# Performance work log

Measured on AMD Instinct MI355X. Metric: run time of the kernel, lower is better.

## Reference

```python
import jax, jax.numpy as jnp
import numpy as np

STEPS_PER_DAY = 144
HEADS = 4
MODEL_D = 152  # 24 input + 24 tod + 24 dow + 80 adaptive
HEAD_D = MODEL_D // HEADS
FF_D = 256
L = 12
PRED = 12
N = 358
B = 16
EVT_D = 1024
HID_EVT = 256
NUM_EVT = 4096
KMAX = 8
NEG = -1e30


def _layer_norm(x, g, b, eps=1e-5):
    m = jnp.mean(x, -1, keepdims=True)
    v = jnp.mean((x - m) ** 2, -1, keepdims=True)
    return (x - m) * jax.lax.rsqrt(v + eps) * g + b


def _mha(x, Wq, bq, Wk, bk, Wv, bv, Wo, bo):
    # x: (B, A, S, D); self-attention over axis S
    b_, a_, s_, d_ = x.shape
    q = (x @ Wq + bq).reshape(b_, a_, s_, HEADS, HEAD_D)
    k = (x @ Wk + bk).reshape(b_, a_, s_, HEADS, HEAD_D)
    v = (x @ Wv + bv).reshape(b_, a_, s_, HEADS, HEAD_D)
    scores = jnp.einsum('baqhd,bakhd->bahqk', q, k) * (HEAD_D ** -0.5)
    attn = jax.nn.softmax(scores, axis=-1)
    out = jnp.einsum('bahqk,bakhd->baqhd', attn, v).reshape(b_, a_, s_, d_)
    return out @ Wo + bo


def setup_inputs() -> dict:
    key = jax.random.key(0)
    ks = jax.random.split(key, 24)
    f32 = jnp.float32

    def nrm(k, shape, s=0.02):
        return jax.random.normal(k, shape, dtype=f32) * s

    inp = {}
    inp['var_x'] = jax.random.normal(ks[0], (B, L, N, 1), dtype=f32)
    inp['marker_x'] = jax.random.uniform(ks[1], (B, L, N, 4), dtype=f32)
    inp['W_in'] = nrm(ks[2], (3, 24)); inp['b_in'] = jnp.zeros((24,), f32)
    inp['tod_emb'] = nrm(ks[3], (STEPS_PER_DAY, 24))
    inp['dow_emb'] = nrm(ks[4], (7, 24))
    inp['adaptive_emb'] = nrm(ks[5], (L, N, 80))
    inp['Wq'] = nrm(ks[6], (6, MODEL_D, MODEL_D)); inp['bq'] = jnp.zeros((6, MODEL_D), f32)
    inp['Wk'] = nrm(ks[7], (6, MODEL_D, MODEL_D)); inp['bk'] = jnp.zeros((6, MODEL_D), f32)
    inp['Wv'] = nrm(ks[8], (6, MODEL_D, MODEL_D)); inp['bv'] = jnp.zeros((6, MODEL_D), f32)
    inp['Wo'] = nrm(ks[9], (6, MODEL_D, MODEL_D)); inp['bo'] = jnp.zeros((6, MODEL_D), f32)
    inp['W1'] = nrm(ks[10], (6, MODEL_D, FF_D)); inp['b1'] = jnp.zeros((6, FF_D), f32)
    inp['W2'] = nrm(ks[11], (6, FF_D, MODEL_D)); inp['b2'] = jnp.zeros((6, MODEL_D), f32)
    inp['ln1_g'] = jnp.ones((6, MODEL_D), f32); inp['ln1_b'] = jnp.zeros((6, MODEL_D), f32)
    inp['ln2_g'] = jnp.ones((6, MODEL_D), f32); inp['ln2_b'] = jnp.zeros((6, MODEL_D), f32)
    inp['event_embeddings'] = nrm(ks[12], (NUM_EVT + 1, EVT_D)).at[0].set(0.0)
    inp['W_evt'] = nrm(ks[13], (EVT_D, HID_EVT)); inp['b_evt'] = jnp.zeros((HID_EVT,), f32)
    inp['W_mm'] = nrm(ks[14], (L * (MODEL_D + HID_EVT), PRED)); inp['b_mm'] = jnp.zeros((PRED,), f32)
    inp['W_ts'] = nrm(ks[15], (L * MODEL_D, PRED)); inp['b_ts'] = jnp.zeros((PRED,), f32)
    inp['doy_indices'] = jax.random.randint(ks[16], (366, KMAX), 1, NUM_EVT + 1, dtype=jnp.int32)
    mask = jax.random.uniform(ks[17], (366, KMAX)) < 0.6
    inp['doy_mask'] = mask.at[:, 0].set(True)
    return inp


def reference(var_x, marker_x, W_in, b_in, tod_emb, dow_emb, adaptive_emb,
              Wq, bq, Wk, bk, Wv, bv, Wo, bo, W1, b1, W2, b2,
              ln1_g, ln1_b, ln2_g, ln2_b, event_embeddings, W_evt, b_evt,
              W_mm, b_mm, W_ts, b_ts, doy_indices, doy_mask):
    b_, l_, n_, _ = var_x.shape
    tod = jnp.clip((marker_x[..., 0] * STEPS_PER_DAY).astype(jnp.int32), 0, STEPS_PER_DAY - 1)
    dow = jnp.clip((marker_x[..., 1] * 7).astype(jnp.int32), 0, 6)
    x_in = jnp.concatenate([var_x, marker_x[..., 0:1], marker_x[..., 1:2]], axis=-1)
    x = jnp.concatenate([
        x_in @ W_in + b_in,
        tod_emb[tod],
        dow_emb[dow],
        jnp.broadcast_to(adaptive_emb[None], (b_, l_, n_, adaptive_emb.shape[-1])),
    ], axis=-1)  # (B, L, N, MODEL_D)
    # 3 temporal attention layers (over L), then 3 spatial (over N)
    for i in range(6):
        temporal = i < 3
        h = jnp.swapaxes(x, 1, 2) if temporal else x
        out = _mha(h, Wq[i], bq[i], Wk[i], bk[i], Wv[i], bv[i], Wo[i], bo[i])
        h = _layer_norm(h + out, ln1_g[i], ln1_b[i])
        ff = jax.nn.relu(h @ W1[i] + b1[i]) @ W2[i] + b2[i]
        h = _layer_norm(h + ff, ln2_g[i], ln2_b[i])
        x = jnp.swapaxes(h, 1, 2) if temporal else h
    ts_emb = jnp.swapaxes(x, 1, 2)  # (B, N, L, D)
    # ragged event gather + linear + masked max-pool (one vectorized pass)
    doy = jnp.clip((marker_x[:, -1, 0, 3] * 365).astype(jnp.int32), 0, 365)
    idx = doy_indices[doy]           # (B, KMAX)
    msk = doy_mask[doy]              # (B, KMAX)
    h_evt = event_embeddings[idx] @ W_evt + b_evt  # (B, KMAX, HID_EVT)
    evt = jnp.max(jnp.where(msk[..., None], h_evt, NEG), axis=1)  # (B, HID_EVT)
    evt_b = jnp.broadcast_to(evt[:, None, None, :], (b_, n_, l_, HID_EVT))
    fused = jnp.concatenate([evt_b, ts_emb], axis=-1).reshape(b_, n_, -1)
    mm_pred = fused @ W_mm + b_mm
    ts_pred = ts_emb.reshape(b_, n_, -1) @ W_ts + b_ts
    return jnp.swapaxes(mm_pred + ts_pred, 1, 2)  # (B, PRED, N)
```

## Files before the change

### kernel.cpp

```cpp
#include <hip/hip_runtime.h>
#include <hip/hip_bf16.h>

using bf = __hip_bfloat16;

#define B_   16
#define L_   12
#define N_   358
#define D_   152
#define TOK_ (B_*L_*N_)
#define FF_  256
#define HD_  38
#define SCALE_ 0.16222142113076254f
#define C2_   0.23403921469340696f

__device__ __forceinline__ float bf2f(bf x) { return __bfloat162float(x); }
__device__ __forceinline__ bf f2bf(float f) { return __float2bfloat16(f); }
__device__ __forceinline__ float lo_bf(unsigned u) { return __uint_as_float(u << 16); }
__device__ __forceinline__ float hi_bf(unsigned u) { return __uint_as_float(u & 0xffff0000u); }
__device__ __forceinline__ unsigned pk_bf(float a, float b) {
  union { bf h; unsigned short u; } A, Bu;
  A.h = f2bf(a); Bu.h = f2bf(b);
  return ((unsigned)Bu.u << 16) | A.u;
}

using short8  = __attribute__((ext_vector_type(8))) short;
using float4v = __attribute__((ext_vector_type(4))) float;

__device__ __forceinline__ void gl_lds16(const void* g, void* l) {
  __builtin_amdgcn_global_load_lds(
      (const __attribute__((address_space(1))) void*)g,
      (__attribute__((address_space(3))) void*)l, 16, 0, 0);
}

template<int SUBCB>
__device__ __forceinline__ void issue_w8(const char* gsrc, ushort* lds, int w, int lane) {
  constexpr int TB = SUBCB >> 10;
  constexpr int TAIL = SUBCB & 1023;
#pragma unroll
  for (int blk0 = 0; blk0 < TB; blk0 += 8) {
    int blk = blk0 + w;
    if (blk < TB)
      gl_lds16(gsrc + blk*1024 + (size_t)lane*16, (char*)lds + blk*1024);
  }
  if (TAIL) {
    if (w == (TB & 7) && lane < TAIL/16)
      gl_lds16(gsrc + TB*1024 + (size_t)lane*16, (char*)lds + TB*1024);
  }
}

__device__ __forceinline__ short8 ld_g8(const ushort* p) {
  union { unsigned u[4]; short8 v; } t;
  t.u[0] = *(const unsigned*)(p);
  t.u[1] = *(const unsigned*)(p + 2);
  t.u[2] = *(const unsigned*)(p + 4);
  t.u[3] = *(const unsigned*)(p + 6);
  return t.v;
}

__global__ void k_beacon(float* out, int n, float val) {
  int i = blockIdx.x * 256 + threadIdx.x;
  if (i < n) out[i] = val;
}

__global__ __launch_bounds__(256) void k_embed2(
    const float* __restrict__ var_x, const float* __restrict__ marker,
    const float* __restrict__ W_in, const float* __restrict__ b_in,
    const float* __restrict__ tod_emb, const float* __restrict__ dow_emb,
    const float* __restrict__ adap, bf* __restrict__ x) {
  int t = blockIdx.x * 256 + threadIdx.x;
  if (t >= TOK_) return;
  int n = t % N_;
  int l = (t / N_) % L_;
  float var = var_x[t];
  float m0 = marker[t*4 + 0];
  float m1 = marker[t*4 + 1];
  int tod = (int)(m0 * 144.f); tod = tod < 0 ? 0 : (tod > 143 ? 143 : tod);
  int dw  = (int)(m1 * 7.f);   dw  = dw  < 0 ? 0 : (dw  > 6   ? 6   : dw);
  bf* xp = x + (long)t * D_;
  for (int d = 0; d < 24; ++d)
    xp[d] = f2bf(var * W_in[d] + m0 * W_in[24 + d] + m1 * W_in[48 + d] + b_in[d]);
  for (int d = 0; d < 24; ++d) xp[24 + d] = f2bf(tod_emb[tod*24 + d]);
  for (int d = 0; d < 24; ++d) xp[48 + d] = f2bf(dow_emb[dw*24 + d]);
  for (int d = 0; d < 80; ++d) xp[72 + d] = f2bf(adap[(l*N_ + n)*80 + d]);
}

__global__ __launch_bounds__(256) void k_wprep6(
    const float* __restrict__ Wq, const float* __restrict__ Wk,
    const float* __restrict__ Wv, const float* __restrict__ Wo,
    const float* __restrict__ W1, const float* __restrict__ W2,
    unsigned* __restrict__ out) {
  int i = blockIdx.x * 256 + threadIdx.x;
  if (i >= 6*115200) return;
  int layer = i / 115200, r = i % 115200;
  const float* src; int K, Nd, d, up, c;
  if (r < 48000) {
    c = r / 9600; int rr = r % 9600; int m = rr / 3200; int r2 = rr % 3200;
    d = r2 / 20; up = r2 % 20;
    src = (m == 0 ? Wq : (m == 1 ? Wk : Wv)) + layer*23104; K = 152; Nd = 152;
  } else if (r < 64000) {
    int rr = r - 48000; c = rr / 3200; int r2 = rr % 3200;
    d = r2 / 20; up = r2 % 20;
    src = Wo + layer*23104; K = 152; Nd = 152;
  } else if (r < 89600) {
    int rr = r - 64000; c = rr / 5120; int r2 = rr % 5120;
    d = r2 / 20; up = r2 % 20;
    src = W1 + layer*38912; K = 152; Nd = 256;
  } else {
    int rr = r - 89600; c = rr / 3200; int r2 = rr % 3200;
    d = r2 / 20; up = r2 % 20;
    src = W2 + layer*38912; K = 256; Nd = 152;
  }
  float v0 = 0.f, v1 = 0.f;
  int k0 = 32*c + 2*up;
  if (up < 16 && d < Nd) {
    if (k0 < K)     v0 = src[(long)k0*Nd + d];
    if (k0 + 1 < K) v1 = src[(long)(k0+1)*Nd + d];
  }
  out[i] = pk_bf(v0, v1);
}

template<int K, int Nd, int NW, int TOKB, int CSPLIT, bool RELU, bool LN>
__global__ __launch_bounds__(512) void k_gemm7(
    const bf* __restrict__ X, const ushort* __restrict__ Wg,
    const float* __restrict__ bi0, const float* __restrict__ bi1,
    const float* __restrict__ bi2, const bf* __restrict__ Res,
    const float* __restrict__ g, const float* __restrict__ bb,
    bf* __restrict__ Y0, bf* __restrict__ Y1, bf* __restrict__ Y2) {
  constexpr int NJ   = (Nd + 15) / 16;
  constexpr int NdP  = NJ * 16;
  constexpr int KC   = (K + 31) / 32;
  constexpr int G    = NW * CSPLIT;
  constexpr int S    = KC * G;
  constexpr int IR   = NdP / CSPLIT;
  constexpr int SUB_USH = IR * 40;
  constexpr int SUBCB   = SUB_USH * 2;
  constexpr int NJW  = IR / 32;
  constexpr int MR   = TOKB / 64;
  constexpr bool GLX = (K == 152);
  constexpr int XSTR = GLX ? K : (K + 8);
  __shared__ __align__(16) ushort Xs[TOKB * XSTR + 8];
  __shared__ __align__(16) ushort Wb[2 * SUB_USH];
  long row0 = (long)blockIdx.x * TOKB;
  int tid = threadIdx.x;
  int lane = tid & 63, w = tid >> 6;
  int cl = lane & 15, gr = lane >> 4;
  int wr = w >> 1, wc = w & 1;
  if constexpr (GLX) {
    constexpr int TBX = TOKB * K * 2 / 1024;
    const char* Xgc = (const char*)(X + row0 * K);
#pragma unroll
    for (int b0 = 0; b0 < TBX; b0 += 8) {
      int blk = b0 + w;
      if (blk < TBX)
        gl_lds16(Xgc + blk*1024 + (size_t)lane*16, (char*)Xs + blk*1024);
    }
  } else {
    const char* Xgc = (const char*)(X + row0 * K);
    for (int i = tid; i < TOKB*(K/8); i += 512) {
      int r = i / (K/8), c = i % (K/8);
      *(short8*)&Xs[r*XSTR + 8*c] = *(const short8*)(Xgc + r*(K*2) + c*16);
    }
  }
  const char* gW = (const char*)Wg;
  issue_w8<SUBCB>(gW, Wb, w, lane);
  __syncthreads();
  float4v acc[G][MR][NJW];
#pragma unroll
  for (int gi = 0; gi < G; ++gi)
#pragma unroll
    for (int mi = 0; mi < MR; ++mi)
#pragma unroll
      for (int j = 0; j < NJW; ++j) acc[gi][mi][j] = (float4v){0.f,0.f,0.f,0.f};
#pragma unroll
  for (int s = 0; s < S; ++s) {
    if (s + 1 < S)
      issue_w8<SUBCB>(gW + (size_t)(s+1)*SUBCB, Wb + ((s+1)&1)*SUB_USH, w, lane);
    int kc = (s / G) * 32;
    const ushort* wb = Wb + (s&1)*SUB_USH;
    short8 af[MR];
#pragma unroll
    for (int mi = 0; mi < MR; ++mi)
      af[mi] = *(const short8*)&Xs[((TOKB/4)*wr + 16*mi + cl)*XSTR + kc + 8*gr];
#pragma unroll
    for (int j = 0; j < NJW; ++j) {
      short8 bv = *(const short8*)&wb[((IR/2)*wc + 16*j + cl)*40 + 8*gr];
#pragma unroll
      for (int mi = 0; mi < MR; ++mi)
        acc[s % G][mi][j] =
            __builtin_amdgcn_mfma_f32_16x16x32_bf16(af[mi], bv, acc[s % G][mi][j], 0, 0, 0);
    }
    __syncthreads();
  }
  if constexpr (!LN) {
#pragma unroll
    for (int gi = 0; gi < G; ++gi) {
      bf* Y = (NW > 1) ? (gi == 0 ? Y0 : (gi == 1 ? Y1 : Y2)) : Y0;
      const float* bp = (NW > 1) ? (gi == 0 ? bi0 : (gi == 1 ? bi1 : bi2)) : bi0;
      int colb = (CSPLIT > 1 ? IR*gi : 0) + (IR/2)*wc;
#pragma unroll
      for (int j = 0; j < NJW; ++j) {
        int col = colb + 16*j + cl;
        if (col < Nd) {
          float bvs = bp[col];
#pragma unroll
          for (int mi = 0; mi < MR; ++mi) {
            long rw = row0 + (TOKB/4)*wr + 16*mi + 4*gr;
#pragma unroll
            for (int r = 0; r < 4; ++r) {
              float val = acc[gi][mi][j][r] + bvs;
              if (RELU) val = fmaxf(val, 0.f);
              Y[(rw + r) * Nd + col] = f2bf(val);
            }
          }
        }
      }
    }
  } else {
    float* LNb = (float*)Wb;
    int colb = (IR/2)*wc;
#pragma unroll
    for (int j = 0; j < NJW; ++j) {
      int col = colb + 16*j + cl;
      if (col < Nd) {
        float bvs = bi0[col];
#pragma unroll
        for (int mi = 0; mi < MR; ++mi) {
          long rw = row0 + (TOKB/4)*wr + 16*mi + 4*gr;
#pragma unroll
          for (int r = 0; r < 4; ++r)
            acc[0][mi][j][r] += bvs + bf2f(Res[(rw + r) * Nd + col]);
        }
      }
    }
    float mean[MR][4], rs[MR][4];
#pragma unroll
    for (int mi = 0; mi < MR; ++mi)
#pragma unroll
      for (int r = 0; r < 4; ++r) {
        float s = 0.f;
#pragma unroll
        for (int j = 0; j < NJW; ++j) s += acc[0][mi][j][r];
        s += __shfl_xor(s, 1, 64); s += __shfl_xor(s, 2, 64);
        s += __shfl_xor(s, 4, 64); s += __shfl_xor(s, 8, 64);
        if (cl == 0) LNb[((wr*MR + mi)*2 + wc)*16 + 4*gr + r] = s;
      }
    __syncthreads();
#pragma unroll
    for (int mi = 0; mi < MR; ++mi)
#pragma unroll
      for (int r = 0; r < 4; ++r) {
        float tot = LNb[((wr*MR + mi)*2 + 0)*16 + 4*gr + r]
                  + LNb[((wr*MR + mi)*2 + 1)*16 + 4*gr + r];
        mean[mi][r] = tot * (1.f / (float)Nd);
      }
#pragma unroll
    for (int mi = 0; mi < MR; ++mi)
#pragma unroll
      for (int r = 0; r < 4; ++r) {
        float s2 = 0.f;
#pragma unroll
        for (int j = 0; j < NJW; ++j) {
          int col = colb + 16*j + cl;
          if (col < Nd) {
            float dv = acc[0][mi][j][r] - mean[mi][r];
            s2 += dv*dv;
          }
        }
        s2 += __shfl_xor(s2, 1, 64); s2 += __shfl_xor(s2, 2, 64);
        s2 += __shfl_xor(s2, 4, 64); s2 += __shfl_xor(s2, 8, 64);
        if (cl == 0) LNb[256 + ((wr*MR + mi)*2 + wc)*16 + 4*gr + r] = s2;
      }
    __syncthreads();
#pragma unroll
    for (int mi = 0; mi < MR; ++mi)
#pragma unroll
      for (int r = 0; r < 4; ++r) {
        float tot2 = LNb[256 + ((wr*MR + mi)*2 + 0)*16 + 4*gr + r]
                   + LNb[256 + ((wr*MR + mi)*2 + 1)*16 + 4*gr + r];
        rs[mi][r] = rsqrtf(tot2 * (1.f / (float)Nd) + 1e-5f);
      }
#pragma unroll
    for (int j = 0; j < NJW; ++j) {
      int col = colb + 16*j + cl;
      if (col < Nd) {
        float gv = g[col], bv2 = bb[col];
#pragma unroll
        for (int mi = 0; mi < MR; ++mi) {
          long rw = row0 + (TOKB/4)*wr + 16*mi + 4*gr;
#pragma unroll
          for (int r = 0; r < 4; ++r)
            Y0[(rw + r) * Nd + col] =
                f2bf((acc[0][mi][j][r] - mean[mi][r]) * rs[mi][r] * gv + bv2);
        }
      }
    }
  }
}

__global__ __launch_bounds__(256) void k_attn_t2(
    const ushort* __restrict__ qg, const ushort* __restrict__ kg,
    const ushort* __restrict__ vg, bf* __restrict__ a) {
  int id = blockIdx.x; int b = id / N_; int n = id % N_;
  __shared__ ushort Ksh[4][16][40];
  __shared__ ushort Qsh[4][16][40];
  __shared__ ushort Vth[4][40][16];
  int tid = threadIdx.x;
  for (int i = tid; i < 1280; i += 256) {
    ((unsigned*)Ksh)[i] = 0u; ((unsigned*)Qsh)[i] = 0u; ((unsigned*)Vth)[i] = 0u;
  }
  __syncthreads();
  for (int i = tid; i < 4*12*19; i += 256) {
    int h = i / 228, r = i % 228, l = r / 19, t2 = r % 19;
    long off = ((long)(b*L_ + l) * N_ + n) * D_ + h*HD_ + 2*t2;
    *(unsigned*)&Ksh[h][l][2*t2] = *(const unsigned*)(kg + off);
    *(unsigned*)&Qsh[h][l][2*t2] = *(const unsigned*)(qg + off);
  }
  for (int i = tid; i < 4*12*19; i += 256) {
    int h = i / 228, r = i % 228, l = r / 19, t2 = r % 19;
    long off = ((long)(b*L_ + l) * N_ + n) * D_ + h*HD_ + 2*t2;
    unsigned u = *(const unsigned*)(vg + off);
    Vth[h][2*t2][l]     = (ushort)(u & 0xffffu);
    Vth[h][2*t2 + 1][l] = (ushort)(u >> 16);
  }
  __syncthreads();
  int lane = tid & 63, w = tid >> 6;
  int cl = lane & 15, gr = lane >> 4;
  const short8 z8 = {0,0,0,0,0,0,0,0};
  short8 a00 = *(const short8*)&Ksh[w][cl][8*gr];
  short8 qB0 = *(const short8*)&Qsh[w][cl][8*gr];
  short8 a01 = (gr == 0) ? *(const short8*)&Ksh[w][cl][32] : z8;
  short8 qB1 = (gr == 0) ? *(const short8*)&Qsh[w][cl][32] : z8;
  float4v sa = (float4v){0,0,0,0};
  sa = __builtin_amdgcn_mfma_f32_16x16x32_bf16(a00, qB0, sa, 0, 0, 0);
  sa = __builtin_amdgcn_mfma_f32_16x16x32_bf16(a01, qB1, sa, 0, 0, 0);
  float p[4];
#pragma unroll
  for (int r = 0; r < 4; ++r) {
    float xv = (4*gr + r < 12) ? sa[r]*C2_ : -1e30f;
    p[r] = __builtin_exp2f(fminf(xv, 80.f));
  }
  float sum_ = (p[0] + p[1]) + (p[2] + p[3]);
  sum_ += __shfl_xor(sum_, 16, 64);
  sum_ += __shfl_xor(sum_, 32, 64);
  unsigned u0 = pk_bf(p[0], p[1]);
  unsigned u1 = pk_bf(p[2], p[3]);
  int srcA = cl + 32*(gr & 1);
  int srcB = srcA + 16;
  unsigned w0 = __shfl(u0, srcA, 64), w1 = __shfl(u1, srcA, 64);
  unsigned w2 = __shfl(u0, srcB, 64), w3 = __shfl(u1, srcB, 64);
  union { unsigned u[4]; short8 v; } pbu;
  bool gv = gr < 2;
  pbu.u[0] = gv ? w0 : 0u; pbu.u[1] = gv ? w1 : 0u;
  pbu.u[2] = gv ? w2 : 0u; pbu.u[3] = gv ? w3 : 0u;
  short8 pB = pbu.v;
  float4v accO[3];
#pragma unroll
  for (int dt = 0; dt < 3; ++dt) {
    short8 aV = (gv && (dt < 2 || cl < 8))
        ? *(const short8*)&Vth[w][16*dt + cl][8*gr] : z8;
    accO[dt] = (float4v){0,0,0,0};
    accO[dt] = __builtin_amdgcn_mfma_f32_16x16x32_bf16(aV, pB, accO[dt], 0, 0, 0);
  }
  if (cl < 12) {
    float inv = 1.f / sum_;
    bf* ap = a + ((long)(b*L_ + cl) * N_ + n) * D_ + w*HD_;
#pragma unroll
    for (int dt = 0; dt < 2; ++dt) {
      *(unsigned*)(ap + 16*dt + 4*gr)     = pk_bf(accO[dt][0]*inv, accO[dt][1]*inv);
      *(unsigned*)(ap + 16*dt + 4*gr + 2) = pk_bf(accO[dt][2]*inv, accO[dt][3]*inv);
    }
    if (gr == 0) {
      *(unsigned*)(ap + 32) = pk_bf(accO[2][0]*inv, accO[2][1]*inv);
      *(unsigned*)(ap + 34) = pk_bf(accO[2][2]*inv, accO[2][3]*inv);
    } else if (gr == 1) {
      *(unsigned*)(ap + 36) = pk_bf(accO[2][0]*inv, accO[2][1]*inv);
    }
  }
}

__global__ __launch_bounds__(512) void k_attn_s6(
    const ushort* __restrict__ qg, const ushort* __restrict__ kg,
    const ushort* __restrict__ vg, bf* __restrict__ a) {
  __shared__ ushort Ks[360][40];
  __shared__ ushort Vt[38][392];
  int tid = threadIdx.x;
  int lane = tid & 63, w = tid >> 6;
  int cl = lane & 15, gr = lane >> 4;
  bool g0 = (gr == 0);
  const short8 z8 = {0,0,0,0,0,0,0,0};

  for (int uu = 0; uu < 2; ++uu) {
    int id = blockIdx.x * 2 + uu;
    int h = id & 3; int s = id >> 2;
    int b = s / L_; int l = s % L_;
    long base = (long)(b*L_ + l) * N_;
    if (uu) __syncthreads();
    for (int i = tid; i < 360*20; i += 512) {
      int j = i / 20, t2 = i % 20;
      unsigned u = 0u;
      if (j < N_ && t2 < 19)
        u = *(const unsigned*)(kg + (base + j)*D_ + h*HD_ + 2*t2);
      *(unsigned*)&Ks[j][2*t2] = u;
    }
    for (int i = tid; i < N_*19; i += 512) {
      int j = i / 19, t2 = i % 19;
      unsigned u = *(const unsigned*)(vg + (base + j)*D_ + h*HD_ + 2*t2);
      Vt[2*t2][j]     = (ushort)(u & 0xffffu);
      Vt[2*t2 + 1][j] = (ushort)(u >> 16);
    }
    for (int i = tid; i < 38*26; i += 512)
      Vt[i / 26][N_ + i % 26] = 0;
    __syncthreads();

    for (int qt = w; qt < 23; qt += 8) {
      const ushort* qp = qg + (base + 16*qt + cl) * D_ + h*HD_;
      short8 qB0 = ld_g8(qp + 8*gr);
      short8 qB1 = ld_g8(qp + 32 + 8*gr);
      float sum_ = 0.f;
      float4v accO[3];
      accO[0] = (float4v){0,0,0,0};
      accO[1] = (float4v){0,0,0,0};
      accO[2] = (float4v){0,0,0,0};
#pragma unroll 1
      for (int pr = 0; pr < 11; ++pr) {
        int k0 = 32*pr;
        int kr0 = k0 + cl;
        int kr1 = k0 + 16 + cl;
        float4v s0a = (float4v){0,0,0,0}, s1a = (float4v){0,0,0,0};
        {
          short8 a00 = *(const short8*)&Ks[kr0][8*gr];
          short8 a10 = *(const short8*)&Ks[kr1][8*gr];
          __builtin_amdgcn_s_setprio(1);
          s0a = __builtin_amdgcn_mfma_f32_16x16x32_bf16(a00, qB0, s0a, 0, 0, 0);
          s1a = __builtin_amdgcn_mfma_f32_16x16x32_bf16(a10, qB0, s1a, 0, 0, 0);
          short8 a01 = g0 ? *(const short8*)&Ks[kr0][32] : z8;
          short8 a11 = g0 ? *(const short8*)&Ks[kr1][32] : z8;
          s0a = __builtin_amdgcn_mfma_f32_16x16x32_bf16(a01, qB1, s0a, 0, 0, 0);
          s1a = __builtin_amdgcn_mfma_f32_16x16x32_bf16(a11, qB1, s1a, 0, 0, 0);
          __builtin_amdgcn_s_setprio(0);
        }
        float p0[4], p1[4];
#pragma unroll
        for (int r = 0; r < 4; ++r) {
          p0[r] = __builtin_exp2f(fminf(s0a[r]*C2_, 80.f));
          p1[r] = __builtin_exp2f(fminf(s1a[r]*C2_, 80.f));
        }
        sum_ += (p0[0] + p0[1]) + (p0[2] + p0[3])
              + (p1[0] + p1[1]) + (p1[2] + p1[3]);
        unsigned u0 = pk_bf(p0[0], p0[1]);
        unsigned u1 = pk_bf(p0[2], p0[3]);
        unsigned u2 = pk_bf(p1[0], p1[1]);
        unsigned u3 = pk_bf(p1[2], p1[3]);
        int srcA = cl + 16*((2*gr) & 3);
        int srcB = srcA + 16;
        unsigned a0 = __shfl(u0, srcA, 64), b0 = __shfl(u1, srcA, 64);
        unsigned c0 = __shfl(u0, srcB, 64), d0 = __shfl(u1, srcB, 64);
        unsigned a2 = __shfl(u2, srcA, 64), b2 = __shfl(u3, srcA, 64);
        unsigned c2 = __shfl(u2, srcB, 64), d2 = __shfl(u3, srcB, 64);
        bool lo = gr < 2;
        union { unsigned u[4]; short8 v; } pbu;
        pbu.u[0] = lo ? a0 : a2;
        pbu.u[1] = lo ? b0 : b2;
        pbu.u[2] = lo ? c0 : c2;
        pbu.u[3] = lo ? d0 : d2;
        short8 pB = pbu.v;
        __builtin_amdgcn_s_setprio(1);
#pragma unroll
        for (int dt = 0; dt < 3; ++dt) {
          short8 aV = (dt < 2 || cl < 6)
              ? *(const short8*)&Vt[16*dt + cl][k0 + 8*gr] : z8;
          accO[dt] = __builtin_amdgcn_mfma_f32_16x16x32_bf16(aV, pB, accO[dt], 0, 0, 0);
        }
        __builtin_amdgcn_s_setprio(0);
      }
      {
        int k0 = 352;
        int kr0 = k0 + cl; if (kr0 > 359) kr0 = 359;
        float4v s0a = (float4v){0,0,0,0};
        {
          short8 a00 = *(const short8*)&Ks[kr0][8*gr];
          s0a = __builtin_amdgcn_mfma_f32_16x16x32_bf16(a00, qB0, s0a, 0, 0, 0);
          short8 a01 = g0 ? *(const short8*)&Ks[kr0][32] : z8;
          s0a = __builtin_amdgcn_mfma_f32_16x16x32_bf16(a01, qB1, s0a, 0, 0, 0);
        }
        float p0[4];
#pragma unroll
        for (int r = 0; r < 4; ++r) {
          float xv = (4*gr + r < 6) ? s0a[r]*C2_ : -1e30f;
          p0[r] = __builtin_exp2f(fminf(xv, 80.f));
        }
        sum_ += (p0[0] + p0[1]) + (p0[2] + p0[3]);
        unsigned u0 = pk_bf(p0[0], p0[1]);
        unsigned u1 = pk_bf(p0[2], p0[3]);
        int srcA = cl + 16*((2*gr) & 3);
        int srcB = srcA + 16;
        unsigned a0 = __shfl(u0, srcA, 64), b0 = __shfl(u1, srcA, 64);
        unsigned c0 = __shfl(u0, srcB, 64), d0 = __shfl(u1, srcB, 64);
        bool lo = gr < 2;
        union { unsigned u[4]; short8 v; } pbu;
        pbu.u[0] = lo ? a0 : 0u;
        pbu.u[1] = lo ? b0 : 0u;
        pbu.u[2] = lo ? c0 : 0u;
        pbu.u[3] = lo ? d0 : 0u;
        short8 pB = pbu.v;
#pragma unroll
        for (int dt = 0; dt < 3; ++dt) {
          short8 aV = (dt < 2 || cl < 6)
              ? *(const short8*)&Vt[16*dt + cl][k0 + 8*gr] : z8;
          accO[dt] = __builtin_amdgcn_mfma_f32_16x16x32_bf16(aV, pB, accO[dt], 0, 0, 0);
        }
      }
      sum_ += __shfl_xor(sum_, 16, 64);
      sum_ += __shfl_xor(sum_, 32, 64);
      int qi = 16*qt + cl;
      if (qi < N_) {
        float inv = 1.f / sum_;
        bf* ap = a + (base + qi)*D_ + h*HD_;
#pragma unroll
        for (int dt = 0; dt < 2; ++dt) {
          *(unsigned*)(ap + 16*dt + 4*gr)     = pk_bf(accO[dt][0]*inv, accO[dt][1]*inv);
          *(unsigned*)(ap + 16*dt + 4*gr + 2) = pk_bf(accO[dt][2]*inv, accO[dt][3]*inv);
        }
        if (gr == 0) {
          *(unsigned*)(ap + 32) = pk_bf(accO[2][0]*inv, accO[2][1]*inv);
          *(unsigned*)(ap + 34) = pk_bf(accO[2][2]*inv, accO[2][3]*inv);
        } else if (gr == 1) {
          *(unsigned*)(ap + 36) = pk_bf(accO[2][0]*inv, accO[2][1]*inv);
        }
      }
    }
  }
}

__global__ __launch_bounds__(256) void k_wcomb(
    const float* __restrict__ W_mm, const float* __restrict__ W_ts,
    float* __restrict__ wcomb, float* __restrict__ wevtsum) {
  int i = blockIdx.x * 256 + threadIdx.x;
  if (i < 1824*12) {
    int r = i / 12, p = i % 12, l = r / 152, d = r % 152;
    wcomb[i] = W_mm[(l*408 + 256 + d)*12 + p] + W_ts[i];
  }
  if (i < 256*12) {
    int e = i / 12, p = i % 12;
    float s = 0.f;
    for (int l = 0; l < 12; ++l) s += W_mm[(l*408 + e)*12 + p];
    wevtsum[i] = s;
  }
}

__global__ __launch_bounds__(256) void k_evt1(
    const float* __restrict__ marker, const int* __restrict__ doy_idx,
    const float* __restrict__ emb, const float* __restrict__ W_evt,
    const float* __restrict__ b_evt, float* __restrict__ evt_h) {
  int bk = blockIdx.x; int b = bk >> 3; int ks = bk & 7;
  float m3 = marker[((b*L_ + (L_-1))*N_ + 0)*4 + 3];
  int doy = (int)(m3 * 365.f); doy = doy < 0 ? 0 : (doy > 365 ? 365 : doy);
  int idx = doy_idx[doy*8 + ks];
  if (idx < 0 || idx > 4096) idx = 0;
  int d = threadIdx.x;
  float acc = b_evt[d];
  const float* er = emb + (long)idx * 1024;
  for (int e = 0; e < 1024; ++e)
    acc += er[e] * W_evt[e*256 + d];
  evt_h[bk*256 + d] = acc;
}

__global__ __launch_bounds__(256) void k_evtpool(
    const float* __restrict__ marker, const void* __restrict__ doy_mask,
    const float* __restrict__ evt_h, float* __restrict__ evtp) {
  __shared__ int hasF32, hasBig;
  if (threadIdx.x == 0) { hasF32 = 0; hasBig = 0; }
  __syncthreads();
  const unsigned* mw = (const unsigned*)doy_mask;
  for (int w = threadIdx.x; w < 732; w += 256) {
    unsigned u = mw[w];
    if (u == 0x3F800000u) hasF32 = 1;
    else if (u > 1u) hasBig = 1;
  }
  __syncthreads();
  int fmt = hasF32 ? 2 : (hasBig ? 1 : 0);
  int b = blockIdx.x;
  float m3 = marker[((b*L_ + (L_-1))*N_ + 0)*4 + 3];
  int doy = (int)(m3 * 365.f); doy = doy < 0 ? 0 : (doy > 365 ? 365 : doy);
  int j = threadIdx.x;
  float mx = -1e30f;
  for (int kx = 0; kx < 8; ++kx) {
    bool mk;
    if (fmt == 2)      mk = ((const float*)doy_mask)[doy*8 + kx] != 0.f;
    else if (fmt == 1) mk = ((const unsigned char*)doy_mask)[doy*8 + kx] != 0;
    else               mk = ((const int*)doy_mask)[doy*8 + kx] != 0;
    if (mk) mx = fmaxf(mx, evt_h[(b*8 + kx)*256 + j]);
  }
  evtp[b*256 + j] = mx;
}

__global__ __launch_bounds__(192) void k_final3(
    const bf* __restrict__ x, const float* __restrict__ wcomb,
    const float* __restrict__ wevtsum, const float* __restrict__ evtp,
    const float* __restrict__ b_mm, const float* __restrict__ b_ts,
    float* __restrict__ out) {
  int id = blockIdx.x; int b = id / N_; int n = id % N_;
  __shared__ float xs[1824];
  __shared__ float part[16][12];
  int tid = threadIdx.x;
  for (int e = tid; e < 1824; e += 192) {
    int l = e / 152, d = e % 152;
    xs[e] = bf2f(x[((long)(b*L_ + l) * N_ + n) * 152 + d]);
  }
  __syncthreads();
  int g2 = tid / 12, p = tid % 12;
  float acc = 0.f;
  for (int e = g2; e < 1824; e += 16)
    acc += xs[e] * wcomb[e*12 + p];
  part[g2][p] = acc;
  __syncthreads();
  if (tid < 12) {
    float s = b_mm[tid] + b_ts[tid];
    for (int e = 0; e < 256; ++e) s += evtp[b*256 + e] * wevtsum[e*12 + tid];
    for (int gg = 0; gg < 16; ++gg) s += part[gg][tid];
    out[(b*12 + tid) * N_ + n] = s;
  }
}

extern "C" void kernel_launch(void* const* d_in, const int* in_sizes, int n_in,
                              void* d_out, int out_size, void* d_ws, size_t ws_size,
                              hipStream_t stream) {
  static const int expect[32] = {
    68736, 274944, 72, 24, 3456, 168, 343680,
    138624, 912, 138624, 912, 138624, 912, 138624, 912,
    233472, 1536, 233472, 912,
    912, 912, 912, 912,
    4195328, 262144, 256,
    58752, 12, 21888, 12,
    2928, 2928 };
  int nb = (out_size + 255)/256;
  if (n_in != 32) {
    k_beacon<<<nb, 256, 0, stream>>>((float*)d_out, out_size, 998.f);
    return;
  }
  for (int i = 0; i < 32; ++i) {
    if (in_sizes[i] != expect[i]) {
      k_beacon<<<nb, 256, 0, stream>>>((float*)d_out, out_size, 1000.f + i);
      return;
    }
  }
  if (out_size != 68736) {
    k_beacon<<<nb, 256, 0, stream>>>((float*)d_out, out_size, 997.f);
    return;
  }

  const float* var_x  = (const float*)d_in[0];
  const float* marker = (const float*)d_in[1];
  const float* W_in   = (const float*)d_in[2];
  const float* b_in   = (const float*)d_in[3];
  const float* tod    = (const float*)d_in[4];
  const float* dow    = (const float*)d_in[5];
  const float* adap   = (const float*)d_in[6];
  const float* Wq = (const float*)d_in[7];  const float* bq = (const float*)d_in[8];
  const float* Wk = (const float*)d_in[9];  const float* bk = (const float*)d_in[10];
  const float* Wv = (const float*)d_in[11]; const float* bv = (const float*)d_in[12];
  const float* Wo = (const float*)d_in[13]; const float* bo = (const float*)d_in[14];
  const float* W1 = (const float*)d_in[15]; const float* b1 = (const float*)d_in[16];
  const float* W2 = (const float*)d_in[17]; const float* b2 = (const float*)d_in[18];
  const float* g1 = (const float*)d_in[19]; const float* be1 = (const float*)d_in[20];
  const float* g2 = (const float*)d_in[21]; const float* be2 = (const float*)d_in[22];
  const float* emb   = (const float*)d_in[23];
  const float* W_evt = (const float*)d_in[24]; const float* b_evt = (const float*)d_in[25];
  const float* W_mm  = (const float*)d_in[26]; const float* b_mm  = (const float*)d_in[27];
  const float* W_ts  = (const float*)d_in[28]; const float* b_ts  = (const float*)d_in[29];
  const int* doyi = (const int*)d_in[30];
  const void* doym = d_in[31];

  const long TD = (long)TOK_ * D_;
  size_t need = (size_t)TD * 2 * 5
              + (size_t)(32768 + 4096 + 3072 + 21888) * 4
              + 2764800
              + 4096;
  if (ws_size < need) {
    k_beacon<<<nb, 256, 0, stream>>>((float*)d_out, out_size, (float)(ws_size >> 20));
    return;
  }

  bf* x = (bf*)d_ws;
  bf* q = x + TD;
  bf* k = q + TD;
  bf* v = k + TD;
  bf* a = v + TD;
  float* evt_h   = (float*)(a + TD);
  float* evtp    = evt_h + 32768;
  float* wevtsum = evtp + 4096;
  float* wcomb   = wevtsum + 3072;
  ushort* wprep  = (ushort*)(wcomb + 21888);

  k_wprep6<<<2700, 256, 0, stream>>>(Wq, Wk, Wv, Wo, W1, W2, (unsigned*)wprep);
  k_embed2<<<(TOK_ + 255)/256, 256, 0, stream>>>(var_x, marker, W_in, b_in,
                                                 tod, dow, adap, x);
  for (int i = 0; i < 6; ++i) {
    const ushort* pl = wprep + (size_t)i * 230400;
    k_gemm7<152,152,3,64,1,false,false><<<TOK_/64, 512, 0, stream>>>(
        x, pl, bq + i*152, bk + i*152, bv + i*152,
        nullptr, nullptr, nullptr, q, k, v);
    if (i < 3)
      k_attn_t2<<<B_*N_, 256, 0, stream>>>(
          (const ushort*)q, (const ushort*)k, (const ushort*)v, a);
    else
      k_attn_s6<<<B_*L_*2, 512, 0, stream>>>(
          (const ushort*)q, (const ushort*)k, (const ushort*)v, a);
    k_gemm7<152,152,1,128,1,false,true><<<TOK_/128, 512, 0, stream>>>(
        a, pl + 96000, bo + i*152, nullptr, nullptr,
        x, g1 + i*152, be1 + i*152, k, nullptr, nullptr);
    k_gemm7<152,256,1,128,2,true,false><<<TOK_/128, 512, 0, stream>>>(
        k, pl + 128000, b1 + i*256, nullptr, nullptr,
        nullptr, nullptr, nullptr, v, nullptr, nullptr);
    k_gemm7<256,152,1,64,1,false,true><<<TOK_/64, 512, 0, stream>>>(
        v, pl + 179200, b2 + i*152, nullptr, nullptr,
        k, g2 + i*152, be2 + i*152, x, nullptr, nullptr);
  }
  k_evt1<<<16*8, 256, 0, stream>>>(marker, doyi, emb, W_evt, b_evt, evt_h);
  k_evtpool<<<16, 256, 0, stream>>>(marker, doym, evt_h, evtp);
  k_wcomb<<<(1824*12 + 255)/256, 256, 0, stream>>>(W_mm, W_ts, wcomb, wevtsum);
  k_final3<<<B_*N_, 192, 0, stream>>>(x, wcomb, wevtsum, evtp, b_mm, b_ts,
                                      (float*)d_out);
}
```

Before: 1.188 ms.

## Fuse FFN up and down GEMMs into one kernel and merge prep kernels

Adds a fused FFN kernel that computes relu(X W1 + b1) into LDS, then the W2 GEMM with residual add and LayerNorm, so the 256-wide hidden activation never goes to global memory. Merges weight prep, embedding, event projection and output-weight combine into a single launch, and vectorises the bf16 loads in the final projection. This cuts HBM traffic and launch count, at the cost of higher LDS use per block, which may lower occupancy.

```diff
diff --git a/kernel.cpp b/kernel.cpp
--- a/kernel.cpp
+++ b/kernel.cpp
@@ -22,6 +22,9 @@
   A.h = f2bf(a); Bu.h = f2bf(b);
   return ((unsigned)Bu.u << 16) | A.u;
 }
+__device__ __forceinline__ ushort f2bf_u(float f) {
+  union { bf h; ushort u; } t; t.h = f2bf(f); return t.u;
+}
 
 using short8  = __attribute__((ext_vector_type(8))) short;
 using float4v = __attribute__((ext_vector_type(4))) float;
@@ -62,34 +65,18 @@
   if (i < n) out[i] = val;
 }
 
-__global__ __launch_bounds__(256) void k_embed2(
-    const float* __restrict__ var_x, const float* __restrict__ marker,
-    const float* __restrict__ W_in, const float* __restrict__ b_in,
-    const float* __restrict__ tod_emb, const float* __restrict__ dow_emb,
-    const float* __restrict__ adap, bf* __restrict__ x) {
-  int t = blockIdx.x * 256 + threadIdx.x;
-  if (t >= TOK_) return;
-  int n = t % N_;
-  int l = (t / N_) % L_;
-  float var = var_x[t];
-  float m0 = marker[t*4 + 0];
-  float m1 = marker[t*4 + 1];
-  int tod = (int)(m0 * 144.f); tod = tod < 0 ? 0 : (tod > 143 ? 143 : tod);
-  int dw  = (int)(m1 * 7.f);   dw  = dw  < 0 ? 0 : (dw  > 6   ? 6   : dw);
-  bf* xp = x + (long)t * D_;
-  for (int d = 0; d < 24; ++d)
-    xp[d] = f2bf(var * W_in[d] + m0 * W_in[24 + d] + m1 * W_in[48 + d] + b_in[d]);
-  for (int d = 0; d < 24; ++d) xp[24 + d] = f2bf(tod_emb[tod*24 + d]);
-  for (int d = 0; d < 24; ++d) xp[48 + d] = f2bf(dow_emb[dw*24 + d]);
-  for (int d = 0; d < 80; ++d) xp[72 + d] = f2bf(adap[(l*N_ + n)*80 + d]);
-}
-
-__global__ __launch_bounds__(256) void k_wprep6(
+#define WPREP_B 2700
+#define EMB_B   269
+#define EVT_B   128
+#define WC_B    86
+#define PREP_B  (WPREP_B + EMB_B + EVT_B + WC_B)
+
+__device__ void d_wprep(int bid, int tid,
     const float* __restrict__ Wq, const float* __restrict__ Wk,
     const float* __restrict__ Wv, const float* __restrict__ Wo,
     const float* __restrict__ W1, const float* __restrict__ W2,
     unsigned* __restrict__ out) {
-  int i = blockIdx.x * 256 + threadIdx.x;
+  int i = bid * 256 + tid;
   if (i >= 6*115200) return;
   int layer = i / 115200, r = i % 115200;
   const float* src; int K, Nd, d, up, c;
@@ -117,6 +104,81 @@
     if (k0 + 1 < K) v1 = src[(long)(k0+1)*Nd + d];
   }
   out[i] = pk_bf(v0, v1);
+}
+
+__device__ void d_embed(int bid, int tid,
+    const float* __restrict__ var_x, const float* __restrict__ marker,
+    const float* __restrict__ W_in, const float* __restrict__ b_in,
+    const float* __restrict__ tod_emb, const float* __restrict__ dow_emb,
+    const float* __restrict__ adap, bf* __restrict__ x) {
+  int t = bid * 256 + tid;
+  if (t >= TOK_) return;
+  int n = t % N_;
+  int l = (t / N_) % L_;
+  float var = var_x[t];
+  float m0 = marker[t*4 + 0];
+  float m1 = marker[t*4 + 1];
+  int tod = (int)(m0 * 144.f); tod = tod < 0 ? 0 : (tod > 143 ? 143 : tod);
+  int dw  = (int)(m1 * 7.f);   dw  = dw  < 0 ? 0 : (dw  > 6   ? 6   : dw);
+  bf* xp = x + (long)t * D_;
+  for (int d = 0; d < 24; ++d)
+    xp[d] = f2bf(var * W_in[d] + m0 * W_in[24 + d] + m1 * W_in[48 + d] + b_in[d]);
+  for (int d = 0; d < 24; ++d) xp[24 + d] = f2bf(tod_emb[tod*24 + d]);
+  for (int d = 0; d < 24; ++d) xp[48 + d] = f2bf(dow_emb[dw*24 + d]);
+  for (int d = 0; d < 80; ++d) xp[72 + d] = f2bf(adap[(l*N_ + n)*80 + d]);
+}
+
+__device__ void d_evt1(int bk, int tid,
+    const float* __restrict__ marker, const int* __restrict__ doy_idx,
+    const float* __restrict__ emb, const float* __restrict__ W_evt,
+    const float* __restrict__ b_evt, float* __restrict__ evt_h) {
+  int b = bk >> 3; int ks = bk & 7;
+  float m3 = marker[((b*L_ + (L_-1))*N_ + 0)*4 + 3];
+  int doy = (int)(m3 * 365.f); doy = doy < 0 ? 0 : (doy > 365 ? 365 : doy);
+  int idx = doy_idx[doy*8 + ks];
+  if (idx < 0 || idx > 4096) idx = 0;
+  int d = tid;
+  float acc = b_evt[d];
+  const float* er = emb + (long)idx * 1024;
+  for (int e = 0; e < 1024; ++e)
+    acc += er[e] * W_evt[e*256 + d];
+  evt_h[bk*256 + d] = acc;
+}
+
+__device__ void d_wcomb(int bid, int tid,
+    const float* __restrict__ W_mm, const float* __restrict__ W_ts,
+    float* __restrict__ wcomb, float* __restrict__ wevtsum) {
+  int i = bid * 256 + tid;
+  if (i < 1824*12) {
+    int r = i / 12, p = i % 12, l = r / 152, d = r % 152;
+    wcomb[i] = W_mm[(l*408 + 256 + d)*12 + p] + W_ts[i];
+  }
+  if (i < 256*12) {
+    int e = i / 12, p = i % 12;
+    float s = 0.f;
+    for (int l = 0; l < 12; ++l) s += W_mm[(l*408 + e)*12 + p];
+    wevtsum[i] = s;
+  }
+}
+
+__global__ __launch_bounds__(256) void k_prep(
+    const float* Wq, const float* Wk, const float* Wv, const float* Wo,
+    const float* W1, const float* W2, unsigned* wout,
+    const float* var_x, const float* marker, const float* W_in,
+    const float* b_in, const float* tod_emb, const float* dow_emb,
+    const float* adap, bf* x,
+    const int* doyi, const float* emb, const float* W_evt,
+    const float* b_evt, float* evt_h,
+    const float* W_mm, const float* W_ts, float* wcomb, float* wevtsum) {
+  int bid = blockIdx.x, tid = threadIdx.x;
+  if (bid < WPREP_B)
+    d_wprep(bid, tid, Wq, Wk, Wv, Wo, W1, W2, wout);
+  else if (bid < WPREP_B + EMB_B)
+    d_embed(bid - WPREP_B, tid, var_x, marker, W_in, b_in, tod_emb, dow_emb, adap, x);
+  else if (bid < WPREP_B + EMB_B + EVT_B)
+    d_evt1(bid - WPREP_B - EMB_B, tid, marker, doyi, emb, W_evt, b_evt, evt_h);
+  else
+    d_wcomb(bid - WPREP_B - EMB_B - EVT_B, tid, W_mm, W_ts, wcomb, wevtsum);
 }
 
 template<int K, int Nd, int NW, int TOKB, int CSPLIT, bool RELU, bool LN>
@@ -297,6 +359,150 @@
   }
 }
 
+__global__ __launch_bounds__(512) void k_ffn(
+    const bf* __restrict__ X, const ushort* __restrict__ W1g,
+    const ushort* __restrict__ W2g,
+    const float* __restrict__ b1, const float* __restrict__ b2,
+    const bf* __restrict__ Res, const float* __restrict__ g,
+    const float* __restrict__ bb, bf* __restrict__ Y) {
+  constexpr int S1 = 10, SUB1 = 5120;
+  constexpr int S2 = 8,  SUB2 = 6400;
+  constexpr int HSTR = 260;
+  __shared__ __align__(16) ushort S_[29440];
+  ushort* Xs  = S_;
+  ushort* W1b = S_ + 9728;
+  ushort* Hs  = S_;
+  ushort* W2b = S_ + 16640;
+  long row0 = (long)blockIdx.x * 64;
+  int tid = threadIdx.x, lane = tid & 63, w = tid >> 6;
+  int cl = lane & 15, gr = lane >> 4;
+  int wr = w >> 1, wc = w & 1;
+  {
+    const char* Xgc = (const char*)(X + row0 * 152);
+#pragma unroll
+    for (int b0 = 0; b0 < 19; b0 += 8) {
+      int blk = b0 + w;
+      if (blk < 19)
+        gl_lds16(Xgc + blk*1024 + (size_t)lane*16, (char*)Xs + blk*1024);
+    }
+  }
+  issue_w8<SUB1*2>((const char*)W1g, W1b, w, lane);
+  __syncthreads();
+  float4v acc1[2][4];
+#pragma unroll
+  for (int g2 = 0; g2 < 2; ++g2)
+#pragma unroll
+    for (int j = 0; j < 4; ++j) acc1[g2][j] = (float4v){0.f,0.f,0.f,0.f};
+#pragma unroll
+  for (int s = 0; s < S1; ++s) {
+    if (s + 1 < S1)
+      issue_w8<SUB1*2>((const char*)W1g + (size_t)(s+1)*SUB1*2,
+                       W1b + ((s+1)&1)*SUB1, w, lane);
+    int kc = (s / 2) * 32;
+    const ushort* wb = W1b + (s&1)*SUB1;
+    short8 af = *(const short8*)&Xs[(16*wr + cl)*152 + kc + 8*gr];
+#pragma unroll
+    for (int j = 0; j < 4; ++j) {
+      short8 bv = *(const short8*)&wb[(64*wc + 16*j + cl)*40 + 8*gr];
+      acc1[s&1][j] =
+          __builtin_amdgcn_mfma_f32_16x16x32_bf16(af, bv, acc1[s&1][j], 0, 0, 0);
+    }
+    __syncthreads();
+  }
+#pragma unroll
+  for (int g2 = 0; g2 < 2; ++g2)
+#pragma unroll
+    for (int j = 0; j < 4; ++j) {
+      int col = g2*128 + 64*wc + 16*j + cl;
+      float bvs = b1[col];
+#pragma unroll
+      for (int r = 0; r < 4; ++r) {
+        int row = 16*wr + 4*gr + r;
+        Hs[row*HSTR + col] = f2bf_u(fmaxf(acc1[g2][j][r] + bvs, 0.f));
+      }
+    }
+  issue_w8<SUB2*2>((const char*)W2g, W2b, w, lane);
+  __syncthreads();
+  float4v acc2[5];
+#pragma unroll
+  for (int j = 0; j < 5; ++j) acc2[j] = (float4v){0.f,0.f,0.f,0.f};
+#pragma unroll
+  for (int s = 0; s < S2; ++s) {
+    if (s + 1 < S2)
+      issue_w8<SUB2*2>((const char*)W2g + (size_t)(s+1)*SUB2*2,
+                       W2b + ((s+1)&1)*SUB2, w, lane);
+    int kc = s * 32;
+    const ushort* wb = W2b + (s&1)*SUB2;
+    short8 af = *(const short8*)&Hs[(16*wr + cl)*HSTR + kc + 8*gr];
+#pragma unroll
+    for (int j = 0; j < 5; ++j) {
+      short8 bv = *(const short8*)&wb[(80*wc + 16*j + cl)*40 + 8*gr];
+      acc2[j] =
+          __builtin_amdgcn_mfma_f32_16x16x32_bf16(af, bv, acc2[j], 0, 0, 0);
+    }
+    __syncthreads();
+  }
+  float* LNb = (float*)W2b;
+  int colb = 80*wc;
+#pragma unroll
+  for (int j = 0; j < 5; ++j) {
+    int col = colb + 16*j + cl;
+    if (col < D_) {
+      float bvs = b2[col];
+#pragma unroll
+      for (int r = 0; r < 4; ++r)
+        acc2[j][r] += bvs + bf2f(Res[(row0 + 16*wr + 4*gr + r) * D_ + col]);
+    }
+  }
+  float mean[4], rsv[4];
+#pragma unroll
+  for (int r = 0; r < 4; ++r) {
+    float s = 0.f;
+#pragma unroll
+    for (int j = 0; j < 5; ++j)
+      if (colb + 16*j + cl < D_) s += acc2[j][r];
+    s += __shfl_xor(s, 1, 64); s += __shfl_xor(s, 2, 64);
+    s += __shfl_xor(s, 4, 64); s += __shfl_xor(s, 8, 64);
+    if (cl == 0) LNb[(wr*2 + wc)*16 + 4*gr + r] = s;
+  }
+  __syncthreads();
+#pragma unroll
+  for (int r = 0; r < 4; ++r) {
+    float tot = LNb[(wr*2 + 0)*16 + 4*gr + r] + LNb[(wr*2 + 1)*16 + 4*gr + r];
+    mean[r] = tot * (1.f / (float)D_);
+  }
+#pragma unroll
+  for (int r = 0; r < 4; ++r) {
+    float s2 = 0.f;
+#pragma unroll
+    for (int j = 0; j < 5; ++j) {
+      int col = colb + 16*j + cl;
+      if (col < D_) { float dv = acc2[j][r] - mean[r]; s2 += dv*dv; }
+    }
+    s2 += __shfl_xor(s2, 1, 64); s2 += __shfl_xor(s2, 2, 64);
+    s2 += __shfl_xor(s2, 4, 64); s2 += __shfl_xor(s2, 8, 64);
+    if (cl == 0) LNb[128 + (wr*2 + wc)*16 + 4*gr + r] = s2;
+  }
+  __syncthreads();
+#pragma unroll
+  for (int r = 0; r < 4; ++r) {
+    float tot2 = LNb[128 + (wr*2 + 0)*16 + 4*gr + r]
+               + LNb[128 + (wr*2 + 1)*16 + 4*gr + r];
+    rsv[r] = rsqrtf(tot2 * (1.f / (float)D_) + 1e-5f);
+  }
+#pragma unroll
+  for (int j = 0; j < 5; ++j) {
+    int col = colb + 16*j + cl;
+    if (col < D_) {
+      float gv = g[col], bv2 = bb[col];
+#pragma unroll
+      for (int r = 0; r < 4; ++r)
+        Y[(row0 + 16*wr + 4*gr + r) * D_ + col] =
+            f2bf((acc2[j][r] - mean[r]) * rsv[r] * gv + bv2);
+    }
+  }
+}
+
 __global__ __launch_bounds__(256) void k_attn_t2(
     const ushort* __restrict__ qg, const ushort* __restrict__ kg,
     const ushort* __restrict__ vg, bf* __restrict__ a) {
@@ -532,39 +738,6 @@
   }
 }
 
-__global__ __launch_bounds__(256) void k_wcomb(
-    const float* __restrict__ W_mm, const float* __restrict__ W_ts,
-    float* __restrict__ wcomb, float* __restrict__ wevtsum) {
-  int i = blockIdx.x * 256 + threadIdx.x;
-  if (i < 1824*12) {
-    int r = i / 12, p = i % 12, l = r / 152, d = r % 152;
-    wcomb[i] = W_mm[(l*408 + 256 + d)*12 + p] + W_ts[i];
-  }
-  if (i < 256*12) {
-    int e = i / 12, p = i % 12;
-    float s = 0.f;
-    for (int l = 0; l < 12; ++l) s += W_mm[(l*408 + e)*12 + p];
-    wevtsum[i] = s;
-  }
-}
-
-__global__ __launch_bounds__(256) void k_evt1(
-    const float* __restrict__ marker, const int* __restrict__ doy_idx,
-    const float* __restrict__ emb, const float* __restrict__ W_evt,
-    const float* __restrict__ b_evt, float* __restrict__ evt_h) {
-  int bk = blockIdx.x; int b = bk >> 3; int ks = bk & 7;
-  float m3 = marker[((b*L_ + (L_-1))*N_ + 0)*4 + 3];
-  int doy = (int)(m3 * 365.f); doy = doy < 0 ? 0 : (doy > 365 ? 365 : doy);
-  int idx = doy_idx[doy*8 + ks];
-  if (idx < 0 || idx > 4096) idx = 0;
-  int d = threadIdx.x;
-  float acc = b_evt[d];
-  const float* er = emb + (long)idx * 1024;
-  for (int e = 0; e < 1024; ++e)
-    acc += er[e] * W_evt[e*256 + d];
-  evt_h[bk*256 + d] = acc;
-}
-
 __global__ __launch_bounds__(256) void k_evtpool(
     const float* __restrict__ marker, const void* __restrict__ doy_mask,
     const float* __restrict__ evt_h, float* __restrict__ evtp) {
@@ -603,9 +776,12 @@
   __shared__ float xs[1824];
   __shared__ float part[16][12];
   int tid = threadIdx.x;
-  for (int e = tid; e < 1824; e += 192) {
-    int l = e / 152, d = e % 152;
-    xs[e] = bf2f(x[((long)(b*L_ + l) * N_ + n) * 152 + d]);
+  for (int e = tid; e < 912; e += 192) {
+    int l = e / 76, du = e % 76;
+    unsigned u = *(const unsigned*)((const ushort*)x +
+        (((long)(b*L_ + l) * N_ + n) * 152 + 2*du));
+    xs[l*152 + 2*du]     = lo_bf(u);
+    xs[l*152 + 2*du + 1] = hi_bf(u);
   }
   __syncthreads();
   int g2 = tid / 12, p = tid % 12;
@@ -692,9 +868,12 @@
   float* wcomb   = wevtsum + 3072;
   ushort* wprep  = (ushort*)(wcomb + 21888);
 
-  k_wprep6<<<2700, 256, 0, stream>>>(Wq, Wk, Wv, Wo, W1, W2, (unsigned*)wprep);
-  k_embed2<<<(TOK_ + 255)/256, 256, 0, stream>>>(var_x, marker, W_in, b_in,
-                                                 tod, dow, adap, x);
+  k_prep<<<PREP_B, 256, 0, stream>>>(
+      Wq, Wk, Wv, Wo, W1, W2, (unsigned*)wprep,
+      var_x, marker, W_in, b_in, tod, dow, adap, x,
+      doyi, emb, W_evt, b_evt, evt_h,
+      W_mm, W_ts, wcomb, wevtsum);
+  k_evtpool<<<16, 256, 0, stream>>>(marker, doym, evt_h, evtp);
   for (int i = 0; i < 6; ++i) {
     const ushort* pl = wprep + (size_t)i * 230400;
     k_gemm7<152,152,3,64,1,false,false><<<TOK_/64, 512, 0, stream>>>(
@@ -709,16 +888,10 @@
     k_gemm7<152,152,1,128,1,false,true><<<TOK_/128, 512, 0, stream>>>(
         a, pl + 96000, bo + i*152, nullptr, nullptr,
         x, g1 + i*152, be1 + i*152, k, nullptr, nullptr);
-    k_gemm7<152,256,1,128,2,true,false><<<TOK_/128, 512, 0, stream>>>(
-        k, pl + 128000, b1 + i*256, nullptr, nullptr,
-        nullptr, nullptr, nullptr, v, nullptr, nullptr);
-    k_gemm7<256,152,1,64,1,false,true><<<TOK_/64, 512, 0, stream>>>(
-        v, pl + 179200, b2 + i*152, nullptr, nullptr,
-        k, g2 + i*152, be2 + i*152, x, nullptr, nullptr);
-  }
-  k_evt1<<<16*8, 256, 0, stream>>>(marker, doyi, emb, W_evt, b_evt, evt_h);
-  k_evtpool<<<16, 256, 0, stream>>>(marker, doym, evt_h, evtp);
-  k_wcomb<<<(1824*12 + 255)/256, 256, 0, stream>>>(W_mm, W_ts, wcomb, wevtsum);
+    k_ffn<<<TOK_/64, 512, 0, stream>>>(
+        k, pl + 128000, pl + 179200, b1 + i*256, b2 + i*152,
+        k, g2 + i*152, be2 + i*152, x);
+  }
   k_final3<<<B_*N_, 192, 0, stream>>>(x, wcomb, wevtsum, evtp, b_mm, b_ts,
                                       (float*)d_out);
 }
```

Result: faster. 1.122 ms (-5.6%).
